# Performance work log

Hardware: AMD Instinct MI355X
Metric: run time of the kernel (lower is better)

The kernel has to match this reference:

```python
import jax, jax.numpy as jnp
import numpy as np

B, WIN, D, H, O, P = 512, 128, 256, 512, 64, 64  # batch, window, input_size, hidden, output, plength


def setup_inputs() -> dict:
    key = jax.random.key(0)
    ks = jax.random.split(key, 14)
    s = 0.05
    return {
        "x": jax.random.normal(ks[0], (B, WIN, D), jnp.float32),
        # AdditiveScore params: V (v_d,), W (v_d, 2H), U (v_d, k_d) with v_d = k_d = D
        "V": jax.random.normal(ks[1], (D,), jnp.float32) * s,
        "W": jax.random.normal(ks[2], (D, 2 * H), jnp.float32) * s,
        "U": jax.random.normal(ks[3], (D, D), jnp.float32) * s,
        # LSTM (1 layer, gate order i,f,g,o): input dim D+O
        "W_ih": jax.random.normal(ks[4], (4 * H, D + O), jnp.float32) * s,
        "W_hh": jax.random.normal(ks[5], (4 * H, H), jnp.float32) * s,
        "b_ih": jax.random.normal(ks[6], (4 * H,), jnp.float32) * s,
        "b_hh": jax.random.normal(ks[7], (4 * H,), jnp.float32) * s,
        # dense: hidden -> output
        "Wd": jax.random.normal(ks[8], (O, H), jnp.float32) * s,
        "bd": jax.random.normal(ks[9], (O,), jnp.float32) * s,
        # context_s / context_c: input -> hidden
        "Ws": jax.random.normal(ks[10], (H, D), jnp.float32) * s,
        "bs": jax.random.normal(ks[11], (H,), jnp.float32) * s,
        "Wc": jax.random.normal(ks[12], (H, D), jnp.float32) * s,
        "bc": jax.random.normal(ks[13], (H,), jnp.float32) * s,
    }


def reference(x, V, W, U, W_ih, W_hh, b_ih, b_hh, Wd, bd, Ws, bs, Wc, bc):
    # initial decoder state from last encoder step
    h0 = jnp.tanh(x[:, -1] @ Ws.T + bs)            # (B, H)
    c0 = jax.nn.sigmoid(x[:, -1] @ Wc.T + bc)      # (B, H)
    y0 = jnp.zeros((x.shape[0], bd.shape[0]), x.dtype)
    # U*k is constant across decode steps: precompute once
    Uk = jnp.einsum('vd,bwd->bvw', U, x)

    def step(carry, _):
        h, c, y = carry
        q = jnp.concatenate([h, c], axis=-1)        # (B, 2H)
        Wq = q @ W.T                                # (B, D)
        # e = V^T tanh(Wq + Uk); softmax over window
        score = jnp.einsum('v,bvw->bw', V, jnp.tanh(Wq[:, :, None] + Uk))
        att = jax.nn.softmax(score, axis=-1)
        ctx = jnp.einsum('bw,bwd->bd', att, x)      # (B, D)
        inp = jnp.concatenate([y, ctx], axis=-1)    # (B, O+D)
        gates = inp @ W_ih.T + h @ W_hh.T + b_ih + b_hh
        i_, f_, g_, o_ = jnp.split(gates, 4, axis=-1)
        c_new = jax.nn.sigmoid(f_) * c + jax.nn.sigmoid(i_) * jnp.tanh(g_)
        h_new = jax.nn.sigmoid(o_) * jnp.tanh(c_new)
        y_new = h_new @ Wd.T + bd                   # (B, O)
        return (h_new, c_new, y_new), (y_new, att)

    _, (ys, atts) = jax.lax.scan(step, (h0, c0, y0), None, length=P)
    predict_y = jnp.transpose(ys, (1, 0, 2))        # (B, P, O)
    weight = jnp.transpose(atts, (1, 0, 2))
    return predict_y, weight
```

## Files before the change

### kernel.cpp

```cpp
#include <hip/hip_runtime.h>
#include <hip/hip_bf16.h>

#define B_   512
#define WIN_ 128
#define D_   256
#define H_   512
#define O_   64
#define P_   64
#define K2H  1024
#define KG   832
#define NG   2048
#define NSLN 320

typedef __attribute__((ext_vector_type(8))) short bf16x8;
typedef __attribute__((ext_vector_type(4))) float f32x4;
using bf16 = __hip_bfloat16;

__device__ __forceinline__ float fast_tanh(float x){
    float e = __expf(2.f * x);
    return 1.f - __fdividef(2.f, e + 1.f);
}
__device__ __forceinline__ float fast_sig(float x){
    return __fdividef(1.f, 1.f + __expf(-x));
}
__device__ __forceinline__ float b_lo(unsigned int u){ return __uint_as_float(u << 16); }
__device__ __forceinline__ float b_hi(unsigned int u){ return __uint_as_float(u & 0xffff0000u); }
__device__ __forceinline__ short f2bs(float v){
    return (short)__builtin_bit_cast(unsigned short, __float2bfloat16(v));
}
__device__ __forceinline__ unsigned int pack2(float a, float b){
    unsigned short sa = __builtin_bit_cast(unsigned short, __float2bfloat16(a));
    unsigned short sb = __builtin_bit_cast(unsigned short, __float2bfloat16(b));
    return (unsigned int)sa | ((unsigned int)sb << 16);
}

__global__ void k_prep(const float* __restrict__ x, const float* __restrict__ W,
                       const float* __restrict__ U, const float* __restrict__ W_ih,
                       const float* __restrict__ W_hh, const float* __restrict__ b_ih,
                       const float* __restrict__ b_hh, const float* __restrict__ Wd,
                       const float* __restrict__ Ws, const float* __restrict__ Wc,
                       bf16* __restrict__ x_bf, bf16* __restrict__ Wcomb,
                       bf16* __restrict__ Wsl, bf16* __restrict__ U_bf,
                       bf16* __restrict__ Wsc, float* __restrict__ bsum)
{
    const long NXv = (long)B_ * WIN_ * D_ / 8;
    const long NWC = (long)NG * KG;
    const long NSL = (long)8 * NSLN * 128;
    const long NU  = (long)D_ * D_;
    const long NWS = (long)K2H * D_;
    const long NB  = NG;
    const long total = NXv + NWC + NSL + NU + NWS + NB;
    for (long i = (long)blockIdx.x * blockDim.x + threadIdx.x; i < total;
         i += (long)gridDim.x * blockDim.x) {
        long j = i;
        if (j < NXv) {
            const float4* xp = (const float4*)x + j * 2;
            float4 a = xp[0], b = xp[1];
            bf16x8 v;
            v[0] = f2bs(a.x); v[1] = f2bs(a.y); v[2] = f2bs(a.z); v[3] = f2bs(a.w);
            v[4] = f2bs(b.x); v[5] = f2bs(b.y); v[6] = f2bs(b.z); v[7] = f2bs(b.w);
            *(bf16x8*)((short*)x_bf + j * 8) = v;
            continue;
        }
        j -= NXv;
        if (j < NWC) {
            long n = j / KG, k = j % KG;
            float v = (k < 320) ? W_ih[n * 320 + k] : W_hh[n * 512 + (k - 320)];
            Wcomb[j] = __float2bfloat16(v); continue;
        }
        j -= NWC;
        if (j < NSL) {
            long by = j / (NSLN * 128);
            long rem = j % (NSLN * 128);
            long n = rem / 128, k = rem % 128;
            float v;
            if (n < 256) v = (k < 64) ? W[n * K2H + by * 64 + k]
                                      : W[n * K2H + 512 + by * 64 + (k - 64)];
            else         v = (k < 64) ? Wd[(n - 256) * H_ + by * 64 + k] : 0.f;
            Wsl[j] = __float2bfloat16(v); continue;
        }
        j -= NSL;
        if (j < NU) { U_bf[j] = __float2bfloat16(U[j]); continue; }
        j -= NU;
        if (j < NWS) {
            long n = j / D_, k = j % D_;
            float v = (n < 512) ? Ws[n * D_ + k] : Wc[(n - 512) * D_ + k];
            Wsc[j] = __float2bfloat16(v); continue;
        }
        j -= NWS;
        bsum[j] = b_ih[j] + b_hh[j];
    }
}

__global__ void __launch_bounds__(256) k_init2(const bf16* __restrict__ x_bf,
                       const bf16* __restrict__ Wsc, const float* __restrict__ bs,
                       const float* __restrict__ bc, bf16* __restrict__ q_buf,
                       bf16* __restrict__ A0, float* __restrict__ c_f32)
{
    int wave = threadIdx.x >> 6, lane = threadIdx.x & 63;
    int m0 = blockIdx.x * 16;
    int n0 = blockIdx.y * 64 + wave * 16;
    int r = lane & 15, ko = (lane >> 4) * 8, rj = (lane >> 4) * 4;
    const short* xp = (const short*)x_bf;
    const short* wp = (const short*)Wsc;
    f32x4 acc = {};
    #pragma unroll
    for (int k0 = 0; k0 < D_; k0 += 32) {
        bf16x8 a  = *(const bf16x8*)(xp + (long)(m0 + r) * (WIN_ * D_) + 127 * D_ + k0 + ko);
        bf16x8 bb = *(const bf16x8*)(wp + (long)(n0 + r) * D_ + k0 + ko);
        acc = __builtin_amdgcn_mfma_f32_16x16x32_bf16(a, bb, acc, 0, 0, 0);
    }
    int n = n0 + r;
    if (n0 < 512) {
        float bias = bs[n];
        #pragma unroll
        for (int j = 0; j < 4; ++j) {
            int b = m0 + rj + j;
            float hv = fast_tanh(acc[j] + bias);
            bf16 hb = __float2bfloat16(hv);
            q_buf[(long)b * K2H + n]   = hb;
            A0[(long)b * KG + 320 + n] = hb;
        }
    } else {
        float bias = bc[n - 512];
        #pragma unroll
        for (int j = 0; j < 4; ++j) {
            int b = m0 + rj + j;
            float cv = fast_sig(acc[j] + bias);
            q_buf[(long)b * K2H + n]        = __float2bfloat16(cv);
            c_f32[(long)b * H_ + (n - 512)] = cv;
        }
    }
}

__global__ void __launch_bounds__(256) k_uk(const bf16* __restrict__ U_bf,
                    const bf16* __restrict__ x_bf, bf16* __restrict__ Uk)
{
    __shared__ __align__(16) short xs[64][264];
    int b  = blockIdx.y;
    int v0 = (blockIdx.x >> 1) * 64;
    int w0 = (blockIdx.x & 1) * 64;
    {
        const short* xg = (const short*)x_bf + (long)b * (WIN_ * D_) + (long)w0 * D_;
        int row = threadIdx.x >> 2, c4 = (threadIdx.x & 3) * 8;
        #pragma unroll
        for (int i = 0; i < 8; ++i)
            *(bf16x8*)(&xs[row][c4 + i * 32]) = *(const bf16x8*)(xg + (long)row * D_ + c4 + i * 32);
    }
    __syncthreads();
    int lane = threadIdx.x & 63;
    int wave = threadIdx.x >> 6;
    int r  = lane & 15;
    int ko = (lane >> 4) * 8;
    const short* Up = (const short*)U_bf + (long)(v0 + wave * 16 + r) * D_;
    f32x4 acc[4] = {};
    #pragma unroll 2
    for (int k0 = 0; k0 < D_; k0 += 32) {
        bf16x8 a = *(const bf16x8*)(Up + k0 + ko);
        #pragma unroll
        for (int f = 0; f < 4; ++f) {
            bf16x8 bb = *(const bf16x8*)(&xs[f * 16 + r][k0 + ko]);
            acc[f] = __builtin_amdgcn_mfma_f32_16x16x32_bf16(a, bb, acc[f], 0, 0, 0);
        }
    }
    bf16* up = Uk + (long)b * (D_ * WIN_);
    int vbase = v0 + wave * 16 + (lane >> 4) * 4;
    #pragma unroll
    for (int f = 0; f < 4; ++f) {
        int w = w0 + f * 16 + r;
        #pragma unroll
        for (int j = 0; j < 4; ++j)
            up[(long)(vbase + j) * WIN_ + w] = __float2bfloat16(acc[f][j]);
    }
}

__global__ void __launch_bounds__(256) k_slab0(const bf16* __restrict__ q_buf,
                     const bf16* __restrict__ Wsl, float* __restrict__ slab)
{
    int bx = blockIdx.x, by = blockIdx.y;
    int wave = threadIdx.x >> 6, lane = threadIdx.x & 63;
    int r = lane & 15, ko = (lane >> 4) * 8, rj = (lane >> 4) * 4;
    int m0 = bx * 16;
    const short* qp = (const short*)q_buf;
    const short* wp = (const short*)Wsl + (long)by * NSLN * 128;
    #pragma unroll
    for (int i = 0; i < 5; ++i) {
        int n0 = (wave * 5 + i) * 16;
        f32x4 acc = {};
        #pragma unroll
        for (int k0 = 0; k0 < 128; k0 += 32) {
            long koff = (k0 < 64) ? (by * 64 + k0) : (512 + by * 64 + (k0 - 64));
            bf16x8 a  = *(const bf16x8*)(qp + (long)(m0 + r) * K2H + koff + ko);
            bf16x8 bb = *(const bf16x8*)(wp + (long)(n0 + r) * 128 + k0 + ko);
            acc = __builtin_amdgcn_mfma_f32_16x16x32_bf16(a, bb, acc, 0, 0, 0);
        }
        int n = n0 + r;
        #pragma unroll
        for (int j = 0; j < 4; ++j)
            slab[((long)by * B_ + m0 + rj + j) * NSLN + n] = acc[j];
    }
}

__global__ void __launch_bounds__(512) k_att(
    const bf16* __restrict__ x_bf, const bf16* __restrict__ Uk,
    const float* __restrict__ slab, const float* __restrict__ V,
    const float* __restrict__ bd, bf16* __restrict__ A_cur,
    float* __restrict__ out_y, float* __restrict__ out_w, int s)
{
    __shared__ float v_s[D_];
    __shared__ float wq_s[D_];
    __shared__ float part[32][136];
    __shared__ float att_s[WIN_];
    __shared__ float cpart[16][264];
    __shared__ float redw[4];

    const int b = blockIdx.x;
    const int t = threadIdx.x;
    const int lane = t & 63;

    if (t < D_) {
        v_s[t] = V[t];
        float wsum = 0.f;
        #pragma unroll
        for (int by = 0; by < 8; ++by)
            wsum += slab[((long)by * B_ + b) * NSLN + t];
        wq_s[t] = wsum;
    } else if (t < D_ + O_) {
        int o = t - D_;
        if (s > 0) {
            float yv = bd[o];
            #pragma unroll
            for (int by = 0; by < 8; ++by)
                yv += slab[((long)by * B_ + b) * NSLN + 256 + o];
            out_y[((long)b * P_ + (s - 1)) * O_ + o] = yv;
            A_cur[(long)b * KG + o] = __float2bfloat16(yv);
        } else {
            A_cur[(long)b * KG + o] = __float2bfloat16(0.f);
        }
    }
    __syncthreads();

    {
        const int w16 = t & 15, vg = t >> 4;
        const uint4* ukp = (const uint4*)((const short*)Uk + (long)b * (D_ * WIN_));
        uint4 u[8];
        #pragma unroll
        for (int i = 0; i < 8; ++i)
            u[i] = ukp[(long)(vg * 8 + i) * 16 + w16];
        float scv[8] = {0.f,0.f,0.f,0.f,0.f,0.f,0.f,0.f};
        #pragma unroll
        for (int i = 0; i < 8; ++i) {
            int v = vg * 8 + i;
            float wqv = wq_s[v], vv = v_s[v];
            scv[0] += vv * fast_tanh(wqv + b_lo(u[i].x));
            scv[1] += vv * fast_tanh(wqv + b_hi(u[i].x));
            scv[2] += vv * fast_tanh(wqv + b_lo(u[i].y));
            scv[3] += vv * fast_tanh(wqv + b_hi(u[i].y));
            scv[4] += vv * fast_tanh(wqv + b_lo(u[i].z));
            scv[5] += vv * fast_tanh(wqv + b_hi(u[i].z));
            scv[6] += vv * fast_tanh(wqv + b_lo(u[i].w));
            scv[7] += vv * fast_tanh(wqv + b_hi(u[i].w));
        }
        #pragma unroll
        for (int j = 0; j < 8; ++j) part[vg][w16 * 8 + j] = scv[j];
    }
    __syncthreads();

    float e = 0.f, scw = 0.f;
    if (t < WIN_) {
        #pragma unroll
        for (int q = 0; q < 32; ++q) scw += part[q][t];
        float m = scw;
        #pragma unroll
        for (int off = 32; off > 0; off >>= 1) m = fmaxf(m, __shfl_xor(m, off));
        if (lane == 0) redw[t >> 6] = m;
    }
    __syncthreads();
    if (t < WIN_) {
        float m = fmaxf(redw[0], redw[1]);
        e = __expf(scw - m);
        float l = e;
        #pragma unroll
        for (int off = 32; off > 0; off >>= 1) l += __shfl_xor(l, off);
        if (lane == 0) redw[2 + (t >> 6)] = l;
    }
    __syncthreads();
    if (t < WIN_) {
        float a = __fdividef(e, redw[2] + redw[3]);
        att_s[t] = a;
        out_w[((long)b * P_ + s) * WIN_ + t] = a;
    }
    __syncthreads();

    {
        const int dg = t & 31, wg = t >> 5;
        const uint4* xp = (const uint4*)((const short*)x_bf + (long)b * (WIN_ * D_));
        uint4 u[8];
        #pragma unroll
        for (int i = 0; i < 8; ++i)
            u[i] = xp[(long)(wg * 8 + i) * 32 + dg];
        float cacc[8] = {0.f,0.f,0.f,0.f,0.f,0.f,0.f,0.f};
        #pragma unroll
        for (int i = 0; i < 8; ++i) {
            float a = att_s[wg * 8 + i];
            cacc[0] += a * b_lo(u[i].x);
            cacc[1] += a * b_hi(u[i].x);
            cacc[2] += a * b_lo(u[i].y);
            cacc[3] += a * b_hi(u[i].y);
            cacc[4] += a * b_lo(u[i].z);
            cacc[5] += a * b_hi(u[i].z);
            cacc[6] += a * b_lo(u[i].w);
            cacc[7] += a * b_hi(u[i].w);
        }
        #pragma unroll
        for (int j = 0; j < 8; ++j) cpart[wg][dg * 8 + j] = cacc[j];
    }
    __syncthreads();
    if (t < 128) {
        int d = t * 2;
        float f0 = 0.f, f1 = 0.f;
        #pragma unroll
        for (int q = 0; q < 16; ++q) { f0 += cpart[q][d]; f1 += cpart[q][d + 1]; }
        *(unsigned int*)(A_cur + (long)b * KG + O_ + d) = pack2(f0, f1);
    }
}

__global__ void __launch_bounds__(256) k_gates(const bf16* __restrict__ A_in,
                     const bf16* __restrict__ Wcomb, const bf16* __restrict__ Wsl,
                     const float* __restrict__ bsum, float* __restrict__ c_f32,
                     bf16* __restrict__ A_out, float* __restrict__ slab)
{
    __shared__ short lhc[16][136];
    int bx = blockIdx.x, by = blockIdx.y;
    int wave = threadIdx.x >> 6, lane = threadIdx.x & 63;
    int r = lane & 15, ko = (lane >> 4) * 8, rj = (lane >> 4) * 4;
    int m0 = bx * 16;
    int jw = by * 64 + wave * 16;
    const short* ap = (const short*)A_in;
    const short* wp = (const short*)Wcomb;
    f32x4 acc[4] = {};
    long arow = (long)(m0 + r) * KG;
    #pragma unroll 2
    for (int k0 = 0; k0 < KG; k0 += 32) {
        bf16x8 a = *(const bf16x8*)(ap + arow + k0 + ko);
        #pragma unroll
        for (int g = 0; g < 4; ++g) {
            bf16x8 bb = *(const bf16x8*)(wp + (long)(g * H_ + jw + r) * KG + k0 + ko);
            acc[g] = __builtin_amdgcn_mfma_f32_16x16x32_bf16(a, bb, acc[g], 0, 0, 0);
        }
    }
    int jj = jw + r;
    float bi = bsum[jj], bf_ = bsum[H_ + jj], bg = bsum[2*H_ + jj], bo = bsum[3*H_ + jj];
    #pragma unroll
    for (int j = 0; j < 4; ++j) {
        int b = m0 + rj + j;
        float iv = acc[0][j] + bi;
        float fv = acc[1][j] + bf_;
        float gv = acc[2][j] + bg;
        float ov = acc[3][j] + bo;
        float c_old = c_f32[(long)b * H_ + jj];
        float cn = fast_sig(fv) * c_old + fast_sig(iv) * fast_tanh(gv);
        float hn = fast_sig(ov) * fast_tanh(cn);
        c_f32[(long)b * H_ + jj] = cn;
        short hb = f2bs(hn);
        A_out[(long)b * KG + 320 + jj] = __builtin_bit_cast(bf16, (unsigned short)hb);
        lhc[rj + j][wave * 16 + r]      = hb;
        lhc[rj + j][64 + wave * 16 + r] = f2bs(cn);
    }
    __syncthreads();
    const short* wsl = (const short*)Wsl + (long)by * NSLN * 128;
    #pragma unroll
    for (int i = 0; i < 5; ++i) {
        int n0 = (wave * 5 + i) * 16;
        f32x4 pac = {};
        #pragma unroll
        for (int k0 = 0; k0 < 128; k0 += 32) {
            bf16x8 a  = *(const bf16x8*)(&lhc[r][k0 + ko]);
            bf16x8 bb = *(const bf16x8*)(wsl + (long)(n0 + r) * 128 + k0 + ko);
            pac = __builtin_amdgcn_mfma_f32_16x16x32_bf16(a, bb, pac, 0, 0, 0);
        }
        int n = n0 + r;
        #pragma unroll
        for (int j = 0; j < 4; ++j)
            slab[((long)by * B_ + m0 + rj + j) * NSLN + n] = pac[j];
    }
}

__global__ void __launch_bounds__(256) k_yfin(const float* __restrict__ slab,
                     const float* __restrict__ bd, float* __restrict__ out_y)
{
    int b = blockIdx.x * 4 + (threadIdx.x >> 6);
    int o = threadIdx.x & 63;
    float yv = bd[o];
    #pragma unroll
    for (int by = 0; by < 8; ++by)
        yv += slab[((long)by * B_ + b) * NSLN + 256 + o];
    out_y[((long)b * P_ + 63) * O_ + o] = yv;
}

extern "C" void kernel_launch(void* const* d_in, const int* in_sizes, int n_in,
                              void* d_out, int out_size, void* d_ws, size_t ws_size,
                              hipStream_t stream)
{
    const float* x    = (const float*)d_in[0];
    const float* V    = (const float*)d_in[1];
    const float* W    = (const float*)d_in[2];
    const float* U    = (const float*)d_in[3];
    const float* W_ih = (const float*)d_in[4];
    const float* W_hh = (const float*)d_in[5];
    const float* b_ih = (const float*)d_in[6];
    const float* b_hh = (const float*)d_in[7];
    const float* Wd   = (const float*)d_in[8];
    const float* bd   = (const float*)d_in[9];
    const float* Ws   = (const float*)d_in[10];
    const float* bs   = (const float*)d_in[11];
    const float* Wc   = (const float*)d_in[12];
    const float* bc   = (const float*)d_in[13];

    float* out_y = (float*)d_out;
    float* out_w = (float*)d_out + (long)B_ * P_ * O_;

    char* p = (char*)d_ws;
    auto alloc = [&](size_t bytes) { char* r = p; p += (bytes + 255) & ~(size_t)255; return r; };
    bf16*  x_bf  = (bf16*) alloc((size_t)B_ * WIN_ * D_ * 2);
    bf16*  Uk    = (bf16*) alloc((size_t)B_ * D_ * WIN_ * 2);
    bf16*  q_buf = (bf16*) alloc((size_t)B_ * K2H * 2);
    bf16*  A0    = (bf16*) alloc((size_t)B_ * KG * 2);
    bf16*  A1    = (bf16*) alloc((size_t)B_ * KG * 2);
    float* c_f32 = (float*)alloc((size_t)B_ * H_ * 4);
    float* slab  = (float*)alloc((size_t)8 * B_ * NSLN * 4);
    bf16*  Wcomb = (bf16*) alloc((size_t)NG * KG * 2);
    bf16*  Wsl   = (bf16*) alloc((size_t)8 * NSLN * 128 * 2);
    bf16*  U_bf  = (bf16*) alloc((size_t)D_ * D_ * 2);
    bf16*  Wsc   = (bf16*) alloc((size_t)K2H * D_ * 2);
    float* bsum  = (float*)alloc((size_t)NG * 4);
    bf16*  Abuf[2] = { A0, A1 };

    k_prep<<<8192, 256, 0, stream>>>(x, W, U, W_ih, W_hh, b_ih, b_hh, Wd, Ws, Wc,
                                     x_bf, Wcomb, Wsl, U_bf, Wsc, bsum);
    k_init2<<<dim3(32, 16), 256, 0, stream>>>(x_bf, Wsc, bs, bc, q_buf, A0, c_f32);
    k_uk<<<dim3(8, 512), 256, 0, stream>>>(U_bf, x_bf, Uk);
    k_slab0<<<dim3(32, 8), 256, 0, stream>>>(q_buf, Wsl, slab);

    for (int s = 0; s < P_; ++s) {
        k_att<<<512, 512, 0, stream>>>(x_bf, Uk, slab, V, bd,
                                       Abuf[s & 1], out_y, out_w, s);
        k_gates<<<dim3(32, 8), 256, 0, stream>>>(Abuf[s & 1], Wcomb, Wsl, bsum,
                                                 c_f32, Abuf[(s + 1) & 1], slab);
    }
    k_yfin<<<128, 256, 0, stream>>>(slab, bd, out_y);
}
```

Baseline: 2.350 ms.

## Split gates GEMM K across two wave halves and prefetch x in attention

k_gates now runs 512 threads per block and splits the 832-long K reduction between two groups of four waves. The second group's partial sums go through shared memory and are added by the first group before the LSTM cell update, and the slab projection tiles are spread over all 8 waves. This is meant to cut the latency of the serial per-step gates kernel, which launches only 256 blocks. Separately, k_att loads its x tile into registers at kernel entry so the loads overlap the score and softmax phases, at the cost of higher register pressure; launch_bounds(512,4) is added to keep occupancy.

```diff
diff --git a/kernel.cpp b/kernel.cpp
--- a/kernel.cpp
+++ b/kernel.cpp
@@ -201,7 +201,7 @@
     }
 }
 
-__global__ void __launch_bounds__(512) k_att(
+__global__ void __launch_bounds__(512, 4) k_att(
     const bf16* __restrict__ x_bf, const bf16* __restrict__ Uk,
     const float* __restrict__ slab, const float* __restrict__ V,
     const float* __restrict__ bd, bf16* __restrict__ A_cur,
@@ -217,6 +217,15 @@
     const int b = blockIdx.x;
     const int t = threadIdx.x;
     const int lane = t & 63;
+
+    const int dg = t & 31, wg = t >> 5;
+    uint4 xu[8];
+    {
+        const uint4* xp = (const uint4*)((const short*)x_bf + (long)b * (WIN_ * D_));
+        #pragma unroll
+        for (int i = 0; i < 8; ++i)
+            xu[i] = xp[(long)(wg * 8 + i) * 32 + dg];
+    }
 
     if (t < D_) {
         v_s[t] = V[t];
@@ -293,24 +302,18 @@
     __syncthreads();
 
     {
-        const int dg = t & 31, wg = t >> 5;
-        const uint4* xp = (const uint4*)((const short*)x_bf + (long)b * (WIN_ * D_));
-        uint4 u[8];
-        #pragma unroll
-        for (int i = 0; i < 8; ++i)
-            u[i] = xp[(long)(wg * 8 + i) * 32 + dg];
         float cacc[8] = {0.f,0.f,0.f,0.f,0.f,0.f,0.f,0.f};
         #pragma unroll
         for (int i = 0; i < 8; ++i) {
             float a = att_s[wg * 8 + i];
-            cacc[0] += a * b_lo(u[i].x);
-            cacc[1] += a * b_hi(u[i].x);
-            cacc[2] += a * b_lo(u[i].y);
-            cacc[3] += a * b_hi(u[i].y);
-            cacc[4] += a * b_lo(u[i].z);
-            cacc[5] += a * b_hi(u[i].z);
-            cacc[6] += a * b_lo(u[i].w);
-            cacc[7] += a * b_hi(u[i].w);
+            cacc[0] += a * b_lo(xu[i].x);
+            cacc[1] += a * b_hi(xu[i].x);
+            cacc[2] += a * b_lo(xu[i].y);
+            cacc[3] += a * b_hi(xu[i].y);
+            cacc[4] += a * b_lo(xu[i].z);
+            cacc[5] += a * b_hi(xu[i].z);
+            cacc[6] += a * b_lo(xu[i].w);
+            cacc[7] += a * b_hi(xu[i].w);
         }
         #pragma unroll
         for (int j = 0; j < 8; ++j) cpart[wg][dg * 8 + j] = cacc[j];
@@ -325,23 +328,27 @@
     }
 }
 
-__global__ void __launch_bounds__(256) k_gates(const bf16* __restrict__ A_in,
+__global__ void __launch_bounds__(512) k_gates(const bf16* __restrict__ A_in,
                      const bf16* __restrict__ Wcomb, const bf16* __restrict__ Wsl,
                      const float* __restrict__ bsum, float* __restrict__ c_f32,
                      bf16* __restrict__ A_out, float* __restrict__ slab)
 {
     __shared__ short lhc[16][136];
+    __shared__ float pacc[4][4][64][4];
     int bx = blockIdx.x, by = blockIdx.y;
     int wave = threadIdx.x >> 6, lane = threadIdx.x & 63;
+    int w4 = wave & 3, half = wave >> 2;
     int r = lane & 15, ko = (lane >> 4) * 8, rj = (lane >> 4) * 4;
     int m0 = bx * 16;
-    int jw = by * 64 + wave * 16;
+    int jw = by * 64 + w4 * 16;
     const short* ap = (const short*)A_in;
     const short* wp = (const short*)Wcomb;
     f32x4 acc[4] = {};
     long arow = (long)(m0 + r) * KG;
+    const int kbeg = half * 416;
     #pragma unroll 2
-    for (int k0 = 0; k0 < KG; k0 += 32) {
+    for (int kk = 0; kk < 416; kk += 32) {
+        int k0 = kbeg + kk;
         bf16x8 a = *(const bf16x8*)(ap + arow + k0 + ko);
         #pragma unroll
         for (int g = 0; g < 4; ++g) {
@@ -349,29 +356,39 @@
             acc[g] = __builtin_amdgcn_mfma_f32_16x16x32_bf16(a, bb, acc[g], 0, 0, 0);
         }
     }
-    int jj = jw + r;
-    float bi = bsum[jj], bf_ = bsum[H_ + jj], bg = bsum[2*H_ + jj], bo = bsum[3*H_ + jj];
-    #pragma unroll
-    for (int j = 0; j < 4; ++j) {
-        int b = m0 + rj + j;
-        float iv = acc[0][j] + bi;
-        float fv = acc[1][j] + bf_;
-        float gv = acc[2][j] + bg;
-        float ov = acc[3][j] + bo;
-        float c_old = c_f32[(long)b * H_ + jj];
-        float cn = fast_sig(fv) * c_old + fast_sig(iv) * fast_tanh(gv);
-        float hn = fast_sig(ov) * fast_tanh(cn);
-        c_f32[(long)b * H_ + jj] = cn;
-        short hb = f2bs(hn);
-        A_out[(long)b * KG + 320 + jj] = __builtin_bit_cast(bf16, (unsigned short)hb);
-        lhc[rj + j][wave * 16 + r]      = hb;
-        lhc[rj + j][64 + wave * 16 + r] = f2bs(cn);
+    if (half == 1) {
+        #pragma unroll
+        for (int g = 0; g < 4; ++g)
+            #pragma unroll
+            for (int j = 0; j < 4; ++j)
+                pacc[w4][g][lane][j] = acc[g][j];
+    }
+    __syncthreads();
+    if (half == 0) {
+        int jj = jw + r;
+        float bi = bsum[jj], bf_ = bsum[H_ + jj];
+        float bg = bsum[2*H_ + jj], bo = bsum[3*H_ + jj];
+        #pragma unroll
+        for (int j = 0; j < 4; ++j) {
+            int b = m0 + rj + j;
+            float iv = acc[0][j] + pacc[w4][0][lane][j] + bi;
+            float fv = acc[1][j] + pacc[w4][1][lane][j] + bf_;
+            float gv = acc[2][j] + pacc[w4][2][lane][j] + bg;
+            float ov = acc[3][j] + pacc[w4][3][lane][j] + bo;
+            float c_old = c_f32[(long)b * H_ + jj];
+            float cn = fast_sig(fv) * c_old + fast_sig(iv) * fast_tanh(gv);
+            float hn = fast_sig(ov) * fast_tanh(cn);
+            c_f32[(long)b * H_ + jj] = cn;
+            short hb = f2bs(hn);
+            A_out[(long)b * KG + 320 + jj] = __builtin_bit_cast(bf16, (unsigned short)hb);
+            lhc[rj + j][w4 * 16 + r]      = hb;
+            lhc[rj + j][64 + w4 * 16 + r] = f2bs(cn);
+        }
     }
     __syncthreads();
     const short* wsl = (const short*)Wsl + (long)by * NSLN * 128;
-    #pragma unroll
-    for (int i = 0; i < 5; ++i) {
-        int n0 = (wave * 5 + i) * 16;
+    for (int tile = wave; tile < 20; tile += 8) {
+        int n0 = tile * 16;
         f32x4 pac = {};
         #pragma unroll
         for (int k0 = 0; k0 < 128; k0 += 32) {
@@ -445,7 +462,7 @@
     for (int s = 0; s < P_; ++s) {
         k_att<<<512, 512, 0, stream>>>(x_bf, Uk, slab, V, bd,
                                        Abuf[s & 1], out_y, out_w, s);
-        k_gates<<<dim3(32, 8), 256, 0, stream>>>(Abuf[s & 1], Wcomb, Wsl, bsum,
+        k_gates<<<dim3(32, 8), 512, 0, stream>>>(Abuf[s & 1], Wcomb, Wsl, bsum,
                                                  c_f32, Abuf[(s + 1) & 1], slab);
     }
     k_yfin<<<128, 256, 0, stream>>>(slab, bd, out_y);
```

Result: slower. 2.610 ms (+11.0%).
